# Performance work log

Measured on AMD Instinct MI355X. Metric: run time of the kernel, lower is better.

## Reference

```python
import jax, jax.numpy as jnp
import numpy as np

DIM = 100      # number of assets in the basket
M = 50         # time steps
T = 1.0
R = 0.05
SIGMA = 0.2
S0 = 100.0
DT = T / M
H = 128        # hidden_dim of ZetaNetwork
B = 8192       # Monte-Carlo paths (batch)
EPS = 1e-5     # torch LayerNorm eps


def _layernorm(x, g, b):
    mu = jnp.mean(x, axis=-1, keepdims=True)
    var = jnp.mean((x - mu) ** 2, axis=-1, keepdims=True)
    return (x - mu) / jnp.sqrt(var + EPS) * g + b


def setup_inputs() -> dict:
    key = jax.random.key(0)
    ks = jax.random.split(key, 12)
    dw = jax.random.normal(ks[0], (B, M, DIM), dtype=jnp.float32)
    t_grid = jax.random.uniform(ks[1], (B, M), dtype=jnp.float32)
    s = 0.05
    inp = {
        "dw": dw,
        "t_grid": t_grid,
        "W1": jax.random.normal(ks[2], (DIM + 1, H), dtype=jnp.float32) * s,
        "b1": jnp.zeros((H,), jnp.float32),
        "g1": jnp.ones((H,), jnp.float32),
        "be1": jnp.zeros((H,), jnp.float32),
        "W2": jax.random.normal(ks[3], (H, H), dtype=jnp.float32) * s,
        "b2": jnp.zeros((H,), jnp.float32),
        "g2": jnp.ones((H,), jnp.float32),
        "be2": jnp.zeros((H,), jnp.float32),
        "W3": jax.random.normal(ks[4], (H, H), dtype=jnp.float32) * s,
        "b3": jnp.zeros((H,), jnp.float32),
        "g3": jnp.ones((H,), jnp.float32),
        "be3": jnp.zeros((H,), jnp.float32),
        "W4": jax.random.normal(ks[5], (H, DIM), dtype=jnp.float32) * s,
        "b4": jnp.zeros((DIM,), jnp.float32),
        "Y0": jnp.array([10.0], dtype=jnp.float32),
    }
    return inp


def reference(dw, t_grid, W1, b1, g1, be1, W2, b2, g2, be2,
              W3, b3, g3, be3, W4, b4, Y0):
    batch = dw.shape[0]

    def zeta_net(x):  # x: [B, DIM+1]
        h = jax.nn.gelu(_layernorm(x @ W1 + b1, g1, be1), approximate=False)
        h = jax.nn.gelu(_layernorm(h @ W2 + b2, g2, be2), approximate=False)
        h = jax.nn.gelu(_layernorm(h @ W3 + b3, g3, be3), approximate=False)
        return jax.nn.sigmoid(h @ W4 + b4)  # [B, DIM]

    def step(carry, xs):
        S, Y = carry
        dw_i, t_i = xs                                   # [B,DIM], [B,1]
        net_in = jnp.concatenate([S / S0, t_i], axis=1)  # [B,DIM+1]
        zeta = zeta_net(net_in)
        dS = S * (R * DT + SIGMA * dw_i)
        portfolio_gain = jnp.sum(zeta * dS, axis=1, keepdims=True)
        asset_val = jnp.sum(zeta * S, axis=1, keepdims=True)
        Y = Y + R * (Y - asset_val) * DT + portfolio_gain
        S = S + dS
        return (S, Y), None

    S_init = jnp.full((batch, DIM), S0, dtype=dw.dtype)
    Y_init = jnp.ones((batch, 1), dtype=dw.dtype) * Y0
    xs = (jnp.swapaxes(dw, 0, 1),                # [M,B,DIM]
          jnp.swapaxes(t_grid, 0, 1)[..., None])  # [M,B,1]
    (S, Y), _ = jax.lax.scan(step, (S_init, Y_init), xs)
    return (Y, S)
```

## Files before the change

kernel.cpp:

```cpp
#include <hip/hip_runtime.h>
#include <hip/hip_bf16.h>
#include <cstdint>
#include <cstddef>

typedef __attribute__((ext_vector_type(8))) short short8;
typedef __attribute__((ext_vector_type(4))) float f32x4;
typedef __attribute__((ext_vector_type(2))) float f32x2;
typedef __attribute__((ext_vector_type(4))) unsigned int u32x4;

#define NDIM 100
#define NSTEP 50
#define NPATH 8192
#define XSTR 128
#define ESTR 128

typedef const __attribute__((address_space(1))) unsigned int glb_u32;
typedef __attribute__((address_space(3))) unsigned int lds_u32;

__device__ __forceinline__ unsigned short f2b(float f){
  unsigned int u = __float_as_uint(f);
  u += 0x7fffu + ((u >> 16) & 1u);
  return (unsigned short)(u >> 16);
}
__device__ __forceinline__ float b2f(unsigned short h){
  return __uint_as_float(((unsigned int)h) << 16);
}

__global__ __launch_bounds__(256) void prep_weights(
    const float* __restrict__ W1, const float* __restrict__ W2,
    const float* __restrict__ W3, const float* __restrict__ W4,
    unsigned short* __restrict__ WTS)
{
  int idx = blockIdx.x * 256 + threadIdx.x;
  int j = idx & 7;
  int s = (idx >> 3) & 15;
  int n = (idx >> 7) & 127;
  int L = idx >> 14;
  int lc = s ^ (n & 15);
  int k  = j * 16 + lc;
  float v;
  if (L == 0)      v = (k <= NDIM) ? W1[k * 128 + n] : 0.f;
  else if (L == 1) v = W2[k * 128 + n];
  else if (L == 2) v = W3[k * 128 + n];
  else             v = (n < NDIM) ? W4[k * NDIM + n] : 0.f;
  WTS[idx] = f2b(v);
}

__global__ __launch_bounds__(256) void prep_params(
    const float* __restrict__ b1, const float* __restrict__ g1, const float* __restrict__ be1,
    const float* __restrict__ b2, const float* __restrict__ g2, const float* __restrict__ be2,
    const float* __restrict__ b3, const float* __restrict__ g3, const float* __restrict__ be3,
    const float* __restrict__ b4, float* __restrict__ PPAR)
{
  int idx = blockIdx.x * 256 + threadIdx.x;
  if (idx >= 1536) return;
  int ct = idx & 7;
  int c  = (idx >> 3) & 15;
  int p  = (idx >> 7) % 3;
  int L  = idx / 384;
  int col = ct * 16 + c;
  const float* v;
  if (L == 0)      v = (p == 0) ? b1 : (p == 1) ? g1 : be1;
  else if (L == 1) v = (p == 0) ? b2 : (p == 1) ? g2 : be2;
  else if (L == 2) v = (p == 0) ? b3 : (p == 1) ? g3 : be3;
  else             v = b4;
  float val;
  if (L == 3) val = (p == 0 && col < NDIM) ? b4[col] : 0.f;
  else        val = v[col];
  PPAR[idx] = val;
}

__global__ __launch_bounds__(256) void phaseA(
    const float* __restrict__ dw, const float* __restrict__ tg,
    unsigned short* __restrict__ X, unsigned short* __restrict__ E,
    float* __restrict__ Sout, int path0)
{
  const int pb = threadIdx.x >> 6;
  const int t  = threadIdx.x & 63;
  const int bl = blockIdx.x * 4 + pb;
  const int b  = path0 + bl;
  const int d0 = (t & 7) * 16 + (t >> 3);
  const int d1 = d0 + 8;
  float s0 = 100.f, s1 = 100.f;
  const float* dwb = dw + (long)b * NSTEP * NDIM;
  const float* tgb = tg + (long)b * NSTEP;
  unsigned short* Xb = X + (long)bl * NSTEP * XSTR;
  unsigned short* Eb = E + (long)bl * NSTEP * ESTR;
  for (int i = 0; i < NSTEP; ++i){
    float tv = tgb[i];
    float w0 = (d0 < NDIM) ? dwb[i * NDIM + d0] : 0.f;
    float w1 = (d1 < NDIM) ? dwb[i * NDIM + d1] : 0.f;
    unsigned short* Xr = Xb + i * XSTR;
    unsigned short* Er = Eb + i * ESTR;
    Xr[t]      = (d0 < NDIM) ? f2b(s0 * 0.01f) : ((d0 == NDIM) ? f2b(tv) : (unsigned short)0);
    Xr[t + 64] = (d1 < NDIM) ? f2b(s1 * 0.01f) : (unsigned short)0;
    Er[t]      = (d0 < NDIM) ? f2b(0.2f * s0 * w0) : (unsigned short)0;
    Er[t + 64] = (d1 < NDIM) ? f2b(0.2f * s1 * w1) : (unsigned short)0;
    s0 = fmaf(s0, 0.001f + 0.2f * w0, s0);
    s1 = fmaf(s1, 0.001f + 0.2f * w1, s1);
  }
  if (d0 < NDIM) Sout[(long)b * NDIM + d0] = s0;
  if (d1 < NDIM) Sout[(long)b * NDIM + d1] = s1;
}

__global__ __launch_bounds__(512, 4) void phaseB(
    const unsigned short* __restrict__ X,
    const unsigned short* __restrict__ E,
    const unsigned short* __restrict__ WTS,
    const float* __restrict__ PPAR,
    float* __restrict__ cbuf, long row0)
{
  __shared__ __align__(16) char lds[65536];
  char* const wbuf = lds;
  const int tid = threadIdx.x;
  const int w = tid >> 6;
  const int l = tid & 63;
  const int g = l >> 4;
  const int c = l & 15;
  char* const H = lds + 32768 + w * 4096;
  const long base = (long)blockIdx.x * 256 + w * 16;

  auto stage = [&](int Loff){
    #pragma unroll
    for (int it = 0; it < 4; ++it){
      int chunk = it * 8 + w;
      __builtin_amdgcn_global_load_lds((glb_u32*)(WTS + Loff + chunk * 512 + l * 8),
          (lds_u32*)(wbuf + chunk * 1024), 16, 0, 0);
    }
  };

  short8 af0[4], af1[4];
  {
    const unsigned short* xr0 = X + (base + c) * XSTR;
    const unsigned short* xr1 = X + (base + 128 + c) * XSTR;
    #pragma unroll
    for (int ks = 0; ks < 4; ++ks){
      af0[ks] = *(const short8*)(xr0 + 32 * ks + 8 * g);
      af1[ks] = *(const short8*)(xr1 + 32 * ks + 8 * g);
    }
  }

  auto mfma2 = [&](f32x4 (&acc0)[8], f32x4 (&acc1)[8], f32x4 blo, f32x4 bhi){
    #pragma unroll
    for (int ct = 0; ct < 8; ++ct){
      float bs = (ct < 4) ? blo[ct] : bhi[ct - 4];
      f32x4 z; z[0] = bs; z[1] = bs; z[2] = bs; z[3] = bs;
      acc0[ct] = z; acc1[ct] = z;
      const char* rowp = wbuf + ((ct * 16 + c) << 8);
      #pragma unroll
      for (int ks = 0; ks < 4; ++ks){
        short8 bf = *(const short8*)(rowp + (((4 * ks + g) ^ c) << 4));
        acc0[ct] = __builtin_amdgcn_mfma_f32_16x16x32_bf16(af0[ks], bf, acc0[ct], 0, 0, 0);
        acc1[ct] = __builtin_amdgcn_mfma_f32_16x16x32_bf16(af1[ks], bf, acc1[ct], 0, 0, 0);
      }
    }
  };

  auto gelu2 = [&](f32x2 y) -> f32x2 {
    f32x2 a = y * -2.4554673f;
    f32x2 u;
    u[0] = __builtin_amdgcn_exp2f(a[0]);
    u[1] = __builtin_amdgcn_exp2f(a[1]);
    f32x2 d = u + 1.0f;
    f32x2 r;
    r[0] = __builtin_amdgcn_rcpf(d[0]);
    r[1] = __builtin_amdgcn_rcpf(d[1]);
    return y * r;
  };

  auto postproc = [&](f32x4 (&acc)[8], short8 (&af)[4],
                      f32x4 glo, f32x4 ghi, f32x4 belo, f32x4 behi){
    f32x2 sA = {0.f, 0.f}, sB = {0.f, 0.f}, qA = {0.f, 0.f}, qB = {0.f, 0.f};
    #pragma unroll
    for (int ct = 0; ct < 8; ++ct){
      f32x2 xy = __builtin_shufflevector(acc[ct], acc[ct], 0, 1);
      f32x2 zw = __builtin_shufflevector(acc[ct], acc[ct], 2, 3);
      sA += xy; qA += xy * xy;
      sB += zw; qB += zw * zw;
    }
    #pragma unroll
    for (int m = 1; m <= 8; m <<= 1){
      f32x2 t;
      t[0] = __shfl_xor(sA[0], m, 64); t[1] = __shfl_xor(sA[1], m, 64); sA += t;
      t[0] = __shfl_xor(sB[0], m, 64); t[1] = __shfl_xor(sB[1], m, 64); sB += t;
      t[0] = __shfl_xor(qA[0], m, 64); t[1] = __shfl_xor(qA[1], m, 64); qA += t;
      t[0] = __shfl_xor(qB[0], m, 64); t[1] = __shfl_xor(qB[1], m, 64); qB += t;
    }
    f32x2 muA = sA * 0.0078125f, muB = sB * 0.0078125f;
    f32x2 vA = qA * 0.0078125f - muA * muA + 1e-5f;
    f32x2 vB = qB * 0.0078125f - muB * muB + 1e-5f;
    f32x2 rA, rB;
    rA[0] = rsqrtf(vA[0]); rA[1] = rsqrtf(vA[1]);
    rB[0] = rsqrtf(vB[0]); rB[1] = rsqrtf(vB[1]);
    u32x4 ov0, ov1, ov2, ov3;
    #pragma unroll
    for (int p = 0; p < 4; ++p){
      float ga0 = (p < 2) ? glo[2*p]     : ghi[2*p - 4];
      float ga1 = (p < 2) ? glo[2*p + 1] : ghi[2*p - 3];
      float be0 = (p < 2) ? belo[2*p]     : behi[2*p - 4];
      float be1 = (p < 2) ? belo[2*p + 1] : behi[2*p - 3];
      f32x2 xyE = __builtin_shufflevector(acc[2*p],   acc[2*p],   0, 1);
      f32x2 zwE = __builtin_shufflevector(acc[2*p],   acc[2*p],   2, 3);
      f32x2 xyO = __builtin_shufflevector(acc[2*p+1], acc[2*p+1], 0, 1);
      f32x2 zwO = __builtin_shufflevector(acc[2*p+1], acc[2*p+1], 2, 3);
      f32x2 AEA = rA * ga0, AEB = rB * ga0;
      f32x2 AOA = rA * ga1, AOB = rB * ga1;
      f32x2 hEA = gelu2(xyE * AEA + (be0 - muA * AEA));
      f32x2 hEB = gelu2(zwE * AEB + (be0 - muB * AEB));
      f32x2 hOA = gelu2(xyO * AOA + (be1 - muA * AOA));
      f32x2 hOB = gelu2(zwO * AOB + (be1 - muB * AOB));
      unsigned int k0, k1, k2, k3;
      asm("v_cvt_pk_bf16_f32 %0, %1, %2" : "=v"(k0) : "v"(hEA[0]), "v"(hOA[0]));
      asm("v_cvt_pk_bf16_f32 %0, %1, %2" : "=v"(k1) : "v"(hEA[1]), "v"(hOA[1]));
      asm("v_cvt_pk_bf16_f32 %0, %1, %2" : "=v"(k2) : "v"(hEB[0]), "v"(hOB[0]));
      asm("v_cvt_pk_bf16_f32 %0, %1, %2" : "=v"(k3) : "v"(hEB[1]), "v"(hOB[1]));
      ov0[p] = k0; ov1[p] = k1; ov2[p] = k2; ov3[p] = k3;
    }
    int r0 = 4 * g;
    *(u32x4*)(H + (r0 + 0) * 256 + ((c ^ (r0 + 0)) << 4)) = ov0;
    *(u32x4*)(H + (r0 + 1) * 256 + ((c ^ (r0 + 1)) << 4)) = ov1;
    *(u32x4*)(H + (r0 + 2) * 256 + ((c ^ (r0 + 2)) << 4)) = ov2;
    *(u32x4*)(H + (r0 + 3) * 256 + ((c ^ (r0 + 3)) << 4)) = ov3;
    #pragma unroll
    for (int ks = 0; ks < 4; ++ks)
      af[ks] = *(const short8*)(H + c * 256 + (((4 * ks + g) ^ c) << 4));
  };

  auto epilogue = [&](f32x4 (&acc)[8], short8 (&ep)[4], long rbase){
    f32x2 pgA = {0.f, 0.f}, pgB = {0.f, 0.f};
    #pragma unroll
    for (int ct = 0; ct < 8; ++ct){
      f32x2 xy = __builtin_shufflevector(acc[ct], acc[ct], 0, 1);
      f32x2 zw = __builtin_shufflevector(acc[ct], acc[ct], 2, 3);
      f32x2 aA = xy * -1.4426950f, aB = zw * -1.4426950f;
      f32x2 u, d, r;
      u[0] = __builtin_amdgcn_exp2f(aA[0]); u[1] = __builtin_amdgcn_exp2f(aA[1]);
      d = u + 1.f;
      r[0] = __builtin_amdgcn_rcpf(d[0]); r[1] = __builtin_amdgcn_rcpf(d[1]);
      f32x2 eA = { b2f((unsigned short)ep[0][ct]), b2f((unsigned short)ep[1][ct]) };
      pgA += r * eA;
      u[0] = __builtin_amdgcn_exp2f(aB[0]); u[1] = __builtin_amdgcn_exp2f(aB[1]);
      d = u + 1.f;
      r[0] = __builtin_amdgcn_rcpf(d[0]); r[1] = __builtin_amdgcn_rcpf(d[1]);
      f32x2 eB = { b2f((unsigned short)ep[2][ct]), b2f((unsigned short)ep[3][ct]) };
      pgB += r * eB;
    }
    #pragma unroll
    for (int m = 1; m <= 8; m <<= 1){
      f32x2 t;
      t[0] = __shfl_xor(pgA[0], m, 64); t[1] = __shfl_xor(pgA[1], m, 64); pgA += t;
      t[0] = __shfl_xor(pgB[0], m, 64); t[1] = __shfl_xor(pgB[1], m, 64); pgB += t;
    }
    if (c == 0){
      cbuf[row0 + rbase + 4 * g + 0] = pgA[0];
      cbuf[row0 + rbase + 4 * g + 1] = pgA[1];
      cbuf[row0 + rbase + 4 * g + 2] = pgB[0];
      cbuf[row0 + rbase + 4 * g + 3] = pgB[1];
    }
  };

  stage(0);
  __syncthreads();

  #pragma unroll
  for (int L = 0; L < 3; ++L){
    const float* pp = PPAR + L * 384 + c * 8;
    f32x4 blo = *(const f32x4*)pp, bhi = *(const f32x4*)(pp + 4);
    f32x4 acc0[8], acc1[8];
    mfma2(acc0, acc1, blo, bhi);
    f32x4 glo  = *(const f32x4*)(pp + 128), ghi  = *(const f32x4*)(pp + 132);
    f32x4 belo = *(const f32x4*)(pp + 256), behi = *(const f32x4*)(pp + 260);
    __syncthreads();
    stage((L + 1) * 16384);
    postproc(acc0, af0, glo, ghi, belo, behi);
    postproc(acc1, af1, glo, ghi, belo, behi);
    __syncthreads();
  }

  {
    const float* pp = PPAR + 3 * 384 + c * 8;
    f32x4 blo = *(const f32x4*)pp, bhi = *(const f32x4*)(pp + 4);
    short8 ep0[4], ep1[4];
    #pragma unroll
    for (int j = 0; j < 4; ++j){
      ep0[j] = *(const short8*)(E + (base + 4 * g + j) * ESTR + c * 8);
      ep1[j] = *(const short8*)(E + (base + 128 + 4 * g + j) * ESTR + c * 8);
    }
    f32x4 acc0[8], acc1[8];
    mfma2(acc0, acc1, blo, bhi);
    epilogue(acc0, ep0, base);
    epilogue(acc1, ep1, base + 128);
  }
}

__global__ __launch_bounds__(256) void phaseC(const float* __restrict__ cbuf,
                                              const float* __restrict__ Y0,
                                              float* __restrict__ Yout)
{
  int b = blockIdx.x * 256 + threadIdx.x;
  if (b >= NPATH) return;
  const float kk = 1.0f + 0.05f * (1.0f / 50.0f);
  float y = Y0[0];
  const float* cb = cbuf + (long)b * NSTEP;
  #pragma unroll 10
  for (int i = 0; i < NSTEP; ++i) y = y * kk + cb[i];
  Yout[b] = y;
}

extern "C" void kernel_launch(void* const* d_in, const int* in_sizes, int n_in,
                              void* d_out, int out_size, void* d_ws, size_t ws_size,
                              hipStream_t stream)
{
  const float* dw  = (const float*)d_in[0];
  const float* tg  = (const float*)d_in[1];
  const float* W1  = (const float*)d_in[2];
  const float* b1  = (const float*)d_in[3];
  const float* g1  = (const float*)d_in[4];
  const float* be1 = (const float*)d_in[5];
  const float* W2  = (const float*)d_in[6];
  const float* b2  = (const float*)d_in[7];
  const float* g2  = (const float*)d_in[8];
  const float* be2 = (const float*)d_in[9];
  const float* W3  = (const float*)d_in[10];
  const float* b3  = (const float*)d_in[11];
  const float* g3  = (const float*)d_in[12];
  const float* be3 = (const float*)d_in[13];
  const float* W4  = (const float*)d_in[14];
  const float* b4  = (const float*)d_in[15];
  const float* Y0  = (const float*)d_in[16];
  float* out = (float*)d_out;

  char* ws = (char*)d_ws;
  unsigned short* WTS = (unsigned short*)ws;
  float* PPAR = (float*)(ws + 131072);
  float* cbuf = (float*)(ws + 137344);
  char* chunk = ws + 1775744;

  prep_weights<<<256, 256, 0, stream>>>(W1, W2, W3, W4, WTS);
  prep_params<<<6, 256, 0, stream>>>(b1, g1, be1, b2, g2, be2, b3, g3, be3, b4, PPAR);

  long avail = (long)ws_size - 1775744L;
  long pc = (avail > 0) ? (avail / 25600L) : 0;
  if (pc > 8192) pc = 8192;
  pc -= pc % 128;
  if (pc < 128) pc = 128;

  for (long p0 = 0; p0 < 8192; p0 += pc){
    long np = 8192 - p0; if (np > pc) np = pc;
    unsigned short* Xc = (unsigned short*)chunk;
    unsigned short* Ec = Xc + np * 50L * XSTR;
    phaseA<<<(int)(np / 4), 256, 0, stream>>>(dw, tg, Xc, Ec, out + 8192, (int)p0);
    long nrows = np * 50L;
    phaseB<<<(int)(nrows / 256), 512, 0, stream>>>(Xc, Ec, WTS, PPAR, cbuf, p0 * 50L);
  }
  phaseC<<<32, 256, 0, stream>>>(cbuf, Y0, out);
}
```

Measured before the change: 236.3 us.

## Halve phaseB block size and use DPP row reductions for LayerNorm sums

The MLP kernel now runs 256-thread blocks covering 128 rows instead of 512-thread blocks covering 256 rows. LDS drops to 48KB with a 3-block occupancy hint, and weight staging per layer is split over 4 waves doing 8 chunks each. The 16-lane shuffle-xor reductions for the LayerNorm statistics and the epilogue sums are replaced by DPP row_shr adds, which avoid LDS-based shuffles. The trade-off is that weights are staged to LDS twice as many times in total (once per smaller block), which adds global-to-LDS traffic and sync overhead per row.

```diff
diff --git a/kernel.cpp b/kernel.cpp
--- a/kernel.cpp
+++ b/kernel.cpp
@@ -24,6 +24,19 @@
 }
 __device__ __forceinline__ float b2f(unsigned short h){
   return __uint_as_float(((unsigned int)h) << 16);
+}
+
+template<int CTRL>
+__device__ __forceinline__ float dpp_add(float x){
+  int t = __builtin_amdgcn_update_dpp(0, __float_as_int(x), CTRL, 0xF, 0xF, true);
+  return x + __int_as_float(t);
+}
+__device__ __forceinline__ float rowsum16(float x){
+  x = dpp_add<0x128>(x);
+  x = dpp_add<0x124>(x);
+  x = dpp_add<0x122>(x);
+  x = dpp_add<0x121>(x);
+  return x;
 }
 
 __global__ __launch_bounds__(256) void prep_weights(
@@ -103,14 +116,14 @@
   if (d1 < NDIM) Sout[(long)b * NDIM + d1] = s1;
 }
 
-__global__ __launch_bounds__(512, 4) void phaseB(
+__global__ __launch_bounds__(256, 3) void phaseB(
     const unsigned short* __restrict__ X,
     const unsigned short* __restrict__ E,
     const unsigned short* __restrict__ WTS,
     const float* __restrict__ PPAR,
     float* __restrict__ cbuf, long row0)
 {
-  __shared__ __align__(16) char lds[65536];
+  __shared__ __align__(16) char lds[49152];
   char* const wbuf = lds;
   const int tid = threadIdx.x;
   const int w = tid >> 6;
@@ -118,12 +131,12 @@
   const int g = l >> 4;
   const int c = l & 15;
   char* const H = lds + 32768 + w * 4096;
-  const long base = (long)blockIdx.x * 256 + w * 16;
+  const long base = (long)blockIdx.x * 128 + w * 16;
 
   auto stage = [&](int Loff){
     #pragma unroll
-    for (int it = 0; it < 4; ++it){
-      int chunk = it * 8 + w;
+    for (int it = 0; it < 8; ++it){
+      int chunk = w * 8 + it;
       __builtin_amdgcn_global_load_lds((glb_u32*)(WTS + Loff + chunk * 512 + l * 8),
           (lds_u32*)(wbuf + chunk * 1024), 16, 0, 0);
     }
@@ -132,7 +145,7 @@
   short8 af0[4], af1[4];
   {
     const unsigned short* xr0 = X + (base + c) * XSTR;
-    const unsigned short* xr1 = X + (base + 128 + c) * XSTR;
+    const unsigned short* xr1 = X + (base + 64 + c) * XSTR;
     #pragma unroll
     for (int ks = 0; ks < 4; ++ks){
       af0[ks] = *(const short8*)(xr0 + 32 * ks + 8 * g);
@@ -178,14 +191,10 @@
       sA += xy; qA += xy * xy;
       sB += zw; qB += zw * zw;
     }
-    #pragma unroll
-    for (int m = 1; m <= 8; m <<= 1){
-      f32x2 t;
-      t[0] = __shfl_xor(sA[0], m, 64); t[1] = __shfl_xor(sA[1], m, 64); sA += t;
-      t[0] = __shfl_xor(sB[0], m, 64); t[1] = __shfl_xor(sB[1], m, 64); sB += t;
-      t[0] = __shfl_xor(qA[0], m, 64); t[1] = __shfl_xor(qA[1], m, 64); qA += t;
-      t[0] = __shfl_xor(qB[0], m, 64); t[1] = __shfl_xor(qB[1], m, 64); qB += t;
-    }
+    sA[0] = rowsum16(sA[0]); sA[1] = rowsum16(sA[1]);
+    sB[0] = rowsum16(sB[0]); sB[1] = rowsum16(sB[1]);
+    qA[0] = rowsum16(qA[0]); qA[1] = rowsum16(qA[1]);
+    qB[0] = rowsum16(qB[0]); qB[1] = rowsum16(qB[1]);
     f32x2 muA = sA * 0.0078125f, muB = sB * 0.0078125f;
     f32x2 vA = qA * 0.0078125f - muA * muA + 1e-5f;
     f32x2 vB = qB * 0.0078125f - muB * muB + 1e-5f;
@@ -245,12 +254,8 @@
       f32x2 eB = { b2f((unsigned short)ep[2][ct]), b2f((unsigned short)ep[3][ct]) };
       pgB += r * eB;
     }
-    #pragma unroll
-    for (int m = 1; m <= 8; m <<= 1){
-      f32x2 t;
-      t[0] = __shfl_xor(pgA[0], m, 64); t[1] = __shfl_xor(pgA[1], m, 64); pgA += t;
-      t[0] = __shfl_xor(pgB[0], m, 64); t[1] = __shfl_xor(pgB[1], m, 64); pgB += t;
-    }
+    pgA[0] = rowsum16(pgA[0]); pgA[1] = rowsum16(pgA[1]);
+    pgB[0] = rowsum16(pgB[0]); pgB[1] = rowsum16(pgB[1]);
     if (c == 0){
       cbuf[row0 + rbase + 4 * g + 0] = pgA[0];
       cbuf[row0 + rbase + 4 * g + 1] = pgA[1];
@@ -265,7 +270,7 @@
   #pragma unroll
   for (int L = 0; L < 3; ++L){
     const float* pp = PPAR + L * 384 + c * 8;
-    f32x4 blo = *(const f32x4*)pp, bhi = *(const f32x4*)(pp + 4);
+    f32x4 blo  = *(const f32x4*)pp,         bhi  = *(const f32x4*)(pp + 4);
     f32x4 acc0[8], acc1[8];
     mfma2(acc0, acc1, blo, bhi);
     f32x4 glo  = *(const f32x4*)(pp + 128), ghi  = *(const f32x4*)(pp + 132);
@@ -284,12 +289,12 @@
     #pragma unroll
     for (int j = 0; j < 4; ++j){
       ep0[j] = *(const short8*)(E + (base + 4 * g + j) * ESTR + c * 8);
-      ep1[j] = *(const short8*)(E + (base + 128 + 4 * g + j) * ESTR + c * 8);
+      ep1[j] = *(const short8*)(E + (base + 64 + 4 * g + j) * ESTR + c * 8);
     }
     f32x4 acc0[8], acc1[8];
     mfma2(acc0, acc1, blo, bhi);
     epilogue(acc0, ep0, base);
-    epilogue(acc1, ep1, base + 128);
+    epilogue(acc1, ep1, base + 64);
   }
 }
 
@@ -351,7 +356,7 @@
     unsigned short* Ec = Xc + np * 50L * XSTR;
     phaseA<<<(int)(np / 4), 256, 0, stream>>>(dw, tg, Xc, Ec, out + 8192, (int)p0);
     long nrows = np * 50L;
-    phaseB<<<(int)(nrows / 256), 512, 0, stream>>>(Xc, Ec, WTS, PPAR, cbuf, p0 * 50L);
+    phaseB<<<(int)(nrows / 128), 256, 0, stream>>>(Xc, Ec, WTS, PPAR, cbuf, p0 * 50L);
   }
   phaseC<<<32, 256, 0, stream>>>(cbuf, Y0, out);
 }
```

Measured after the change: 201.5 us. 14.7% less time.
